# Performance work log

Hardware: AMD Instinct MI355X
Metric: run time of the kernel (lower is better)

Reference implementation:

```python
import jax, jax.numpy as jnp
import numpy as np

# Static config (matches init_kwargs / docstring example)
SHAPES = ((100, 100), (50, 50), (25, 25), (13, 13))  # (H, W) per level
L, P, NH, HD, E, F = 4, 4, 8, 32, 256, 1024
NUM_LAYERS = 6
EPS = 1e-5
NUM_KEYS = sum(h * w for h, w in SHAPES)  # 13294


def _ln(x, g, b):
    m = jnp.mean(x, -1, keepdims=True)
    v = jnp.var(x, -1, keepdims=True)
    return (x - m) * jax.lax.rsqrt(v + EPS) * g + b


def _ms_deform_attn(value, loc, aw):
    # value: (B,N,NH,HD)  loc: (B,N,NH,L,P,2) normalized  aw: (B,N,NH,L,P)
    B, N = value.shape[:2]
    out = jnp.zeros((B, NH, N, HD), value.dtype)
    start = 0
    for lvl, (h, w) in enumerate(SHAPES):
        v = value[:, start:start + h * w].transpose(0, 2, 1, 3)  # (B,NH,hw,HD)
        start += h * w
        # grid_sample align_corners=False pixel coords
        x = loc[:, :, :, lvl, :, 0] * w - 0.5  # (B,N,NH,P)
        y = loc[:, :, :, lvl, :, 1] * h - 0.5
        x0 = jnp.floor(x); y0 = jnp.floor(y)
        lx = x - x0; ly = y - y0
        x0 = x0.astype(jnp.int32); y0 = y0.astype(jnp.int32)

        def gather(yi, xi):
            valid = ((xi >= 0) & (xi < w) & (yi >= 0) & (yi < h)).astype(value.dtype)
            idx = jnp.clip(yi, 0, h - 1) * w + jnp.clip(xi, 0, w - 1)  # (B,N,NH,P)
            idx = idx.transpose(0, 2, 1, 3).reshape(B, NH, N * P, 1)
            got = jnp.take_along_axis(v, idx, axis=2).reshape(B, NH, N, P, HD)
            return got * valid.transpose(0, 2, 1, 3)[..., None]

        def wgt(a):  # (B,N,NH,P) -> (B,NH,N,P,1)
            return a.transpose(0, 2, 1, 3)[..., None]

        samp = (gather(y0, x0) * wgt((1 - lx) * (1 - ly))
                + gather(y0, x0 + 1) * wgt(lx * (1 - ly))
                + gather(y0 + 1, x0) * wgt((1 - lx) * ly)
                + gather(y0 + 1, x0 + 1) * wgt(lx * ly))  # (B,NH,N,P,HD)
        out = out + jnp.sum(samp * wgt(aw[:, :, :, lvl]), axis=3)
    return out.transpose(0, 2, 1, 3).reshape(B, N, NH * HD)


def _layer(x, ref, Woff, boff, Waw, baw, Wv, bv, Wo, bo, ln1_g, ln1_b, Wf1, bf1, Wf2, bf2, ln2_g, ln2_b):
    B, N, _ = x.shape
    v = (x @ Wv + bv).reshape(B, N, NH, HD)
    off = (x @ Woff + boff).reshape(B, N, NH, L, P, 2)
    aw = jax.nn.softmax((x @ Waw + baw).reshape(B, N, NH, L * P), -1).reshape(B, N, NH, L, P)
    normalizer = jnp.asarray([[w, h] for (h, w) in SHAPES], x.dtype)  # (L,2) in (x,y)=(W,H)
    loc = ref[:, :, None, :, None, :] + off / normalizer[None, None, None, :, None, :]
    attn = _ms_deform_attn(v, loc, aw) @ Wo + bo
    x = _ln(x + attn, ln1_g, ln1_b)
    f = jax.nn.relu(x @ Wf1 + bf1) @ Wf2 + bf2
    return _ln(x + f, ln2_g, ln2_b)


def setup_inputs() -> dict:
    key = jax.random.key(0)
    ks = jax.random.split(key, 10)
    s = 0.02
    return {
        "src": jax.random.normal(ks[0], (2, NUM_KEYS, E), jnp.float32),
        "reference_points": jax.random.uniform(ks[1], (2, NUM_KEYS, L, 2), jnp.float32),
        "spatial_shapes": jnp.asarray(SHAPES, jnp.int32),
        "level_start_index": jnp.asarray([0, 10000, 12500, 13125], jnp.int32),
        "Woff": jax.random.normal(ks[2], (E, NH * L * P * 2), jnp.float32) * s,
        "boff": jnp.zeros((NH * L * P * 2,), jnp.float32),
        "Waw": jax.random.normal(ks[3], (E, NH * L * P), jnp.float32) * s,
        "baw": jnp.zeros((NH * L * P,), jnp.float32),
        "Wv": jax.random.normal(ks[4], (E, E), jnp.float32) * s,
        "bv": jnp.zeros((E,), jnp.float32),
        "Wo": jax.random.normal(ks[5], (E, E), jnp.float32) * s,
        "bo": jnp.zeros((E,), jnp.float32),
        "ln1_g": jnp.ones((E,), jnp.float32),
        "ln1_b": jnp.zeros((E,), jnp.float32),
        "Wf1": jax.random.normal(ks[6], (E, F), jnp.float32) * s,
        "bf1": jnp.zeros((F,), jnp.float32),
        "Wf2": jax.random.normal(ks[7], (F, E), jnp.float32) * s,
        "bf2": jnp.zeros((E,), jnp.float32),
        "ln2_g": jnp.ones((E,), jnp.float32),
        "ln2_b": jnp.zeros((E,), jnp.float32),
    }


def reference(src, reference_points, spatial_shapes, level_start_index, Woff, boff, Waw, baw, Wv, bv, Wo, bo, ln1_g, ln1_b, Wf1, bf1, Wf2, bf2, ln2_g, ln2_b):
    # NOTE: the torch encoder reuses the SAME layer object num_layers times,
    # so parameters are shared across all 6 layers.
    x = src
    for _ in range(NUM_LAYERS):
        x = _layer(x, reference_points, Woff, boff, Waw, baw, Wv, bv, Wo, bo,
                   ln1_g, ln1_b, Wf1, bf1, Wf2, bf2, ln2_g, ln2_b)
    return x
```

## Files before the change

### kernel.cpp

```cpp
#include <hip/hip_runtime.h>
#include <hip/hip_bf16.h>
#include <math.h>

#define NKEYS 13294
#define BATCH 2
#define MROWS (BATCH * NKEYS)
#define EDIM  256
#define FDIM  1024
#define EPSV  1e-5f

typedef __bf16 bf16x8 __attribute__((ext_vector_type(8)));
typedef float  f32x4  __attribute__((ext_vector_type(4)));
typedef float  f32x2  __attribute__((ext_vector_type(2)));

__device__ __forceinline__ void async16(const void* g, void* l) {
    __builtin_amdgcn_global_load_lds(
        (const __attribute__((address_space(1))) void*)g,
        (__attribute__((address_space(3))) void*)l, 16, 0, 0);
}

template<int MODE>
__global__ __launch_bounds__(256, 4) void gemm_mfma_k(
    const __hip_bfloat16* __restrict__ A, const __hip_bfloat16* __restrict__ WT,
    const float* __restrict__ bias, __hip_bfloat16* __restrict__ Cout,
    int M, int N, int K,
    __hip_bfloat16* __restrict__ o_vb, __hip_bfloat16* __restrict__ o_off,
    __hip_bfloat16* __restrict__ o_aw)
{
    constexpr int BM = 128, BN = 128, BKc = 32;
    constexpr int SMX = (BM + BN) * BKc;
    __shared__ __hip_bfloat16 smem[2 * SMX];

    const int gx = gridDim.x, nb = gx * gridDim.y;
    int bxi = blockIdx.x, byi = blockIdx.y;
    if ((nb & 7) == 0) {
        const int id   = byi * gx + bxi;
        const int tile = (id & 7) * (nb >> 3) + (id >> 3);
        bxi = tile % gx; byi = tile / gx;
    }
    const int bm = byi * BM;
    const int bn = bxi * BN;

    const int tid  = threadIdx.x;
    const int lane = tid & 63;
    const int w    = tid >> 6;
    const int wr   = w >> 1, wc = w & 1;
    const int l15  = lane & 15, quad = lane >> 4;

    const int gRow = tid >> 2;
    const int kc8  = (tid & 3) * 8;
    const __hip_bfloat16* gsrc[4];
    int ldsoff[4];
    #pragma unroll
    for (int rr = 0; rr < 4; ++rr) {
        const int gr = gRow + 64 * rr;
        if (gr < BM) {
            int ar = bm + gr; if (ar >= M) ar = M - 1;
            gsrc[rr] = A + (size_t)ar * K + kc8;
        } else {
            gsrc[rr] = WT + (size_t)(bn + gr - BM) * K + kc8;
        }
        ldsoff[rr] = gr * BKc + kc8;
    }

    f32x4 acc[4][4];
    #pragma unroll
    for (int i = 0; i < 4; ++i)
        #pragma unroll
        for (int j = 0; j < 4; ++j) acc[i][j] = (f32x4)0.f;

    const int T = K / BKc;
    #pragma unroll
    for (int rr = 0; rr < 4; ++rr) async16(gsrc[rr], smem + ldsoff[rr]);

    for (int it = 0; it < T; ++it) {
        __syncthreads();
        if (it + 1 < T) {
            const int nxt = ((it + 1) & 1) * SMX;
            const int ko  = (it + 1) * BKc;
            #pragma unroll
            for (int rr = 0; rr < 4; ++rr) async16(gsrc[rr] + ko, smem + nxt + ldsoff[rr]);
        }
        const __hip_bfloat16* sA = smem + (it & 1) * SMX;
        const __hip_bfloat16* sB = sA + BM * BKc;

        bf16x8 a[4], b[4];
        #pragma unroll
        for (int mt = 0; mt < 4; ++mt)
            a[mt] = *(const bf16x8*)&sA[(wr * 64 + mt * 16 + l15) * BKc + quad * 8];
        #pragma unroll
        for (int nt = 0; nt < 4; ++nt)
            b[nt] = *(const bf16x8*)&sB[(wc * 64 + nt * 16 + l15) * BKc + quad * 8];
        #pragma unroll
        for (int mt = 0; mt < 4; ++mt)
            #pragma unroll
            for (int nt = 0; nt < 4; ++nt)
                acc[mt][nt] = __builtin_amdgcn_mfma_f32_16x16x32_bf16(
                    b[nt], a[mt], acc[mt][nt], 0, 0, 0);
    }

    #pragma unroll
    for (int nt = 0; nt < 4; ++nt) {
        const int col = bn + wc * 64 + nt * 16 + quad * 4;
        const float4 bz = *(const float4*)&bias[col];
        #pragma unroll
        for (int mt = 0; mt < 4; ++mt) {
            const int row = bm + wr * 64 + mt * 16 + l15;
            if (row >= M) continue;
            float v0 = acc[mt][nt][0] + bz.x;
            float v1 = acc[mt][nt][1] + bz.y;
            float v2 = acc[mt][nt][2] + bz.z;
            float v3 = acc[mt][nt][3] + bz.w;
            if (MODE == 3) {
                v0 = fmaxf(v0, 0.f); v1 = fmaxf(v1, 0.f);
                v2 = fmaxf(v2, 0.f); v3 = fmaxf(v3, 0.f);
            }
            union { uint2 u; __hip_bfloat16 h[4]; } p;
            p.h[0] = __float2bfloat16(v0); p.h[1] = __float2bfloat16(v1);
            p.h[2] = __float2bfloat16(v2); p.h[3] = __float2bfloat16(v3);
            if (MODE == 1) {
                if (col < 256) {
                    const int bb = (row >= NKEYS) ? 1 : 0;
                    const int hh = col >> 5, d = col & 31;
                    *(uint2*)&o_vb[((size_t)(bb * 7 + hh) * NKEYS + row) * 32 + d] = p.u;
                } else if (col < 512) {
                    *(uint2*)&o_off[(size_t)row * 256 + (col - 256)] = p.u;
                } else {
                    *(uint2*)&o_aw[(size_t)row * 128 + (col - 512)] = p.u;
                }
            } else {
                *(uint2*)&Cout[(size_t)row * N + col] = p.u;
            }
        }
    }
}

template<int FINAL>
__global__ __launch_bounds__(256, 2) void gemm_ln_k(
    const __hip_bfloat16* __restrict__ A, const __hip_bfloat16* __restrict__ WT,
    const float* __restrict__ bias, const __hip_bfloat16* __restrict__ xres,
    const float* __restrict__ g, const float* __restrict__ bta,
    float* __restrict__ xfout, __hip_bfloat16* __restrict__ xbout,
    int M, int K)
{
    constexpr int BM = 64, BN = 256, BKc = 32;
    constexpr int ROWS = BM + BN;
    constexpr int SLAB = ROWS * BKc;
    constexpr int SMX  = 2 * SLAB;
    __shared__ __hip_bfloat16 smem[2 * SMX];

    const int tid  = threadIdx.x;
    const int bm   = blockIdx.x * BM;
    const int lane = tid & 63;
    const int w    = tid >> 6;
    const int l15  = lane & 15, quad = lane >> 4;

    const int gRow = tid >> 2;
    const int kc8  = (tid & 3) * 8;
    const __hip_bfloat16* gsrc[5];
    int ldsoff[5];
    #pragma unroll
    for (int rr = 0; rr < 5; ++rr) {
        const int gr = gRow + 64 * rr;
        if (gr < BM) {
            int ar = bm + gr; if (ar >= M) ar = M - 1;
            gsrc[rr] = A + (size_t)ar * K + kc8;
        } else {
            gsrc[rr] = WT + (size_t)(gr - BM) * K + kc8;
        }
        ldsoff[rr] = gr * BKc + kc8;
    }

    f32x4 acc[4][4];
    #pragma unroll
    for (int i = 0; i < 4; ++i)
        #pragma unroll
        for (int j = 0; j < 4; ++j) acc[i][j] = (f32x4)0.f;

    const int T = K / 64;
    #pragma unroll
    for (int rr = 0; rr < 5; ++rr) {
        async16(gsrc[rr],      smem + ldsoff[rr]);
        async16(gsrc[rr] + 32, smem + SLAB + ldsoff[rr]);
    }

    for (int it = 0; it < T; ++it) {
        __syncthreads();
        if (it + 1 < T) {
            const int nxt = ((it + 1) & 1) * SMX;
            const int ko  = (it + 1) * 64;
            #pragma unroll
            for (int rr = 0; rr < 5; ++rr) {
                async16(gsrc[rr] + ko,      smem + nxt + ldsoff[rr]);
                async16(gsrc[rr] + ko + 32, smem + nxt + SLAB + ldsoff[rr]);
            }
        }
        #pragma unroll
        for (int s = 0; s < 2; ++s) {
            const __hip_bfloat16* sA = smem + (it & 1) * SMX + s * SLAB;
            const __hip_bfloat16* sB = sA + BM * BKc;

            bf16x8 a[4], b[4];
            #pragma unroll
            for (int mt = 0; mt < 4; ++mt)
                a[mt] = *(const bf16x8*)&sA[(mt * 16 + l15) * BKc + quad * 8];
            #pragma unroll
            for (int nt = 0; nt < 4; ++nt)
                b[nt] = *(const bf16x8*)&sB[(w * 64 + nt * 16 + l15) * BKc + quad * 8];
            #pragma unroll
            for (int mt = 0; mt < 4; ++mt)
                #pragma unroll
                for (int nt = 0; nt < 4; ++nt)
                    acc[mt][nt] = __builtin_amdgcn_mfma_f32_16x16x32_bf16(
                        b[nt], a[mt], acc[mt][nt], 0, 0, 0);
        }
    }

    const int colq = w * 64 + quad * 4;

    #pragma unroll
    for (int nt = 0; nt < 4; ++nt) {
        const int col = colq + nt * 16;
        const float4 bz = *(const float4*)&bias[col];
        #pragma unroll
        for (int mt = 0; mt < 4; ++mt) {
            int row = bm + mt * 16 + l15;
            if (row >= M) row = M - 1;
            const ushort4 xr = *(const ushort4*)&xres[(size_t)row * 256 + col];
            acc[mt][nt][0] += bz.x + __uint_as_float((unsigned)xr.x << 16);
            acc[mt][nt][1] += bz.y + __uint_as_float((unsigned)xr.y << 16);
            acc[mt][nt][2] += bz.z + __uint_as_float((unsigned)xr.z << 16);
            acc[mt][nt][3] += bz.w + __uint_as_float((unsigned)xr.w << 16);
        }
    }

    __syncthreads();
    float* stats = (float*)smem;
    #pragma unroll
    for (int mt = 0; mt < 4; ++mt) {
        float s = 0.f, sq = 0.f;
        #pragma unroll
        for (int nt = 0; nt < 4; ++nt)
            #pragma unroll
            for (int r = 0; r < 4; ++r) {
                const float v = acc[mt][nt][r];
                s += v; sq += v * v;
            }
        s  += __shfl_xor(s,  16, 64);  s  += __shfl_xor(s,  32, 64);
        sq += __shfl_xor(sq, 16, 64);  sq += __shfl_xor(sq, 32, 64);
        if (quad == 0) {
            const int rl = mt * 16 + l15;
            stats[(w * 64 + rl) * 2 + 0] = s;
            stats[(w * 64 + rl) * 2 + 1] = sq;
        }
    }
    __syncthreads();

    #pragma unroll
    for (int mt = 0; mt < 4; ++mt) {
        const int rl  = mt * 16 + l15;
        const int row = bm + rl;
        float s  = stats[rl * 2]          + stats[(64 + rl) * 2]
                 + stats[(128 + rl) * 2]  + stats[(192 + rl) * 2];
        float sq = stats[rl * 2 + 1]      + stats[(64 + rl) * 2 + 1]
                 + stats[(128 + rl) * 2 + 1] + stats[(192 + rl) * 2 + 1];
        const float mean = s * (1.f / 256.f);
        const float var  = sq * (1.f / 256.f) - mean * mean;
        const float rstd = rsqrtf(var + EPSV);
        if (row < M) {
            #pragma unroll
            for (int nt = 0; nt < 4; ++nt) {
                const int col = colq + nt * 16;
                const float4 gz  = *(const float4*)&g[col];
                const float4 bb4 = *(const float4*)&bta[col];
                const float v0 = (acc[mt][nt][0] - mean) * rstd * gz.x + bb4.x;
                const float v1 = (acc[mt][nt][1] - mean) * rstd * gz.y + bb4.y;
                const float v2 = (acc[mt][nt][2] - mean) * rstd * gz.z + bb4.z;
                const float v3 = (acc[mt][nt][3] - mean) * rstd * gz.w + bb4.w;
                union { uint2 u; __hip_bfloat16 h[4]; } p;
                p.h[0] = __float2bfloat16(v0); p.h[1] = __float2bfloat16(v1);
                p.h[2] = __float2bfloat16(v2); p.h[3] = __float2bfloat16(v3);
                *(uint2*)&xbout[(size_t)row * 256 + col] = p.u;
                if (FINAL) {
                    float4 f; f.x = v0; f.y = v1; f.z = v2; f.w = v3;
                    *(float4*)&xfout[(size_t)row * 256 + col] = f;
                }
            }
        }
    }
}

#define NB_SRC  6647
#define NB_WV   256
#define NB_WOFF 256
#define NB_WAW  128
#define NB_WO   256
#define NB_WF1  1024
#define NB_WF2  1024
#define NB_BIAS 3
#define NB_PREP (NB_SRC + NB_WV + NB_WOFF + NB_WAW + NB_WO + NB_WF1 + NB_WF2 + NB_BIAS)

__global__ void prep_k(
    const float* __restrict__ src,  __hip_bfloat16* __restrict__ xb,
    const float* __restrict__ Wv,   const float* __restrict__ Woff,
    const float* __restrict__ Waw,  const float* __restrict__ Wo,
    const float* __restrict__ Wf1,  const float* __restrict__ Wf2,
    const float* __restrict__ bv,   const float* __restrict__ boff,
    const float* __restrict__ baw,
    __hip_bfloat16* __restrict__ WT1, __hip_bfloat16* __restrict__ WTo,
    __hip_bfloat16* __restrict__ WTf1, __hip_bfloat16* __restrict__ WTf2,
    float* __restrict__ bias1)
{
    int b = blockIdx.x;
    const int t = threadIdx.x;

    if (b < NB_SRC) {
        const int i = b * 256 + t;
        const float4 v = ((const float4*)src)[i];
        xb[i * 4 + 0] = __float2bfloat16(v.x);
        xb[i * 4 + 1] = __float2bfloat16(v.y);
        xb[i * 4 + 2] = __float2bfloat16(v.z);
        xb[i * 4 + 3] = __float2bfloat16(v.w);
        return;
    }
    b -= NB_SRC;

    const float* W; __hip_bfloat16* WT; int N, rowOff;
    if (b < NB_WV)        { W = Wv;   WT = WT1;  N = 256;  rowOff = 0;   }
    else if ((b -= NB_WV)   < NB_WOFF) { W = Woff; WT = WT1;  N = 256;  rowOff = 256; }
    else if ((b -= NB_WOFF) < NB_WAW)  { W = Waw;  WT = WT1;  N = 128;  rowOff = 512; }
    else if ((b -= NB_WAW)  < NB_WO)   { W = Wo;   WT = WTo;  N = 256;  rowOff = 0;   }
    else if ((b -= NB_WO)   < NB_WF1)  { W = Wf1;  WT = WTf1; N = 1024; rowOff = 0;   }
    else if ((b -= NB_WF1)  < NB_WF2)  { W = Wf2;  WT = WTf2; N = 256;  rowOff = 0;   }
    else {
        b -= NB_WF2;
        const int i = b * 256 + t;
        if (i < 256) bias1[i] = bv[i];
        else if (i < 512) bias1[i] = boff[i - 256];
        else if (i < 640) bias1[i] = baw[i - 512];
        return;
    }
    const int idx = b * 256 + t;
    const int k = idx / N, n = idx % N;
    const int K = (WT == WTf2) ? 1024 : 256;
    WT[(size_t)(rowOff + n) * K + k] = __float2bfloat16(W[idx]);
}

__global__ __launch_bounds__(256) void sample_k(
    const __hip_bfloat16* __restrict__ v_bf,
    const __hip_bfloat16* __restrict__ offb,
    const __hip_bfloat16* __restrict__ awb,
    const float* __restrict__ ref,
    __hip_bfloat16* __restrict__ out)
{
    __shared__ alignas(16) float sw[272][4];
    __shared__ alignas(16) int   sa[272][4];
    const int t  = threadIdx.x;
    const int q0 = blockIdx.x * 2;
    const int qi = t >> 7, h = (t >> 4) & 7;

    {
        const int i = t & 15;
        const int q = q0 + qi;
        const int l = i >> 2;
        const float logit = __bfloat162float(awb[(size_t)q * 128 + h * 16 + i]);
        float mx = logit;
        #pragma unroll
        for (int m = 1; m < 16; m <<= 1) mx = fmaxf(mx, __shfl_xor(mx, m, 64));
        const float e = __expf(logit - mx);
        float s = e;
        #pragma unroll
        for (int m = 1; m < 16; m <<= 1) s += __shfl_xor(s, m, 64);
        const float aw = e / s;

        const int ww = (l == 0) ? 100 : (l == 1) ? 50 : (l == 2) ? 25 : 13;
        const int ls = (l == 0) ? 0 : (l == 1) ? 10000 : (l == 2) ? 12500 : 13125;
        const int b  = (q >= NKEYS) ? 1 : 0;
        const int slab = (b * 8 + h) * NKEYS + ls;

        const __hip_bfloat162 ofp = *(const __hip_bfloat162*)&offb[(size_t)q * 256 + h * 32 + i * 2];
        const float2 rf = *(const float2*)&ref[(size_t)q * 8 + l * 2];
        const float x = rf.x * (float)ww + __bfloat162float(ofp.x) - 0.5f;
        const float y = rf.y * (float)ww + __bfloat162float(ofp.y) - 0.5f;
        const float x0f = floorf(x), y0f = floorf(y);
        const float lx = x - x0f, ly = y - y0f;
        const int x0 = (int)x0f, y0 = (int)y0f;
        const bool x0ok = (x0 >= 0) & (x0 < ww);
        const bool x1ok = (x0 + 1 >= 0) & (x0 + 1 < ww);
        const bool y0ok = (y0 >= 0) & (y0 < ww);
        const bool y1ok = (y0 + 1 >= 0) & (y0 + 1 < ww);

        float w00 = (1.f - lx) * (1.f - ly) * aw;
        float w01 = lx * (1.f - ly) * aw;
        float w10 = (1.f - lx) * ly * aw;
        float w11 = lx * ly * aw;
        int a00 = slab + y0 * ww + x0;
        int a01 = a00 + 1;
        int a10 = a00 + ww;
        int a11 = a10 + 1;
        if (!(y0ok & x0ok)) { w00 = 0.f; a00 = 0; }
        if (!(y0ok & x1ok)) { w01 = 0.f; a01 = 0; }
        if (!(y1ok & x0ok)) { w10 = 0.f; a10 = 0; }
        if (!(y1ok & x1ok)) { w11 = 0.f; a11 = 0; }

        const int idx = (qi * 8 + h) * 17 + i;
        sw[idx][0] = w00; sw[idx][1] = w01; sw[idx][2] = w10; sw[idx][3] = w11;
        sa[idx][0] = a00 * 64; sa[idx][1] = a01 * 64;
        sa[idx][2] = a10 * 64; sa[idx][3] = a11 * 64;
    }
    __syncthreads();

    const int d2 = t & 15;
    const unsigned d4 = d2 * 4;
    const char* vb = (const char*)v_bf;
    const int ebase = (qi * 8 + h) * 17;
    f32x2 acc = (f32x2)0.f;
    #pragma unroll
    for (int i = 0; i < 16; ++i) {
        const f32x4 wv = *(const f32x4*)sw[ebase + i];
        const int4  av = *(const int4*)sa[ebase + i];
        const unsigned p0 = *(const unsigned*)(vb + ((unsigned)av.x + d4));
        const unsigned p1 = *(const unsigned*)(vb + ((unsigned)av.y + d4));
        const unsigned p2 = *(const unsigned*)(vb + ((unsigned)av.z + d4));
        const unsigned p3 = *(const unsigned*)(vb + ((unsigned)av.w + d4));
        f32x2 v;
        v[0] = __uint_as_float(p0 << 16); v[1] = __uint_as_float(p0 & 0xffff0000u);
        acc += (f32x2)(wv[0]) * v;
        v[0] = __uint_as_float(p1 << 16); v[1] = __uint_as_float(p1 & 0xffff0000u);
        acc += (f32x2)(wv[1]) * v;
        v[0] = __uint_as_float(p2 << 16); v[1] = __uint_as_float(p2 & 0xffff0000u);
        acc += (f32x2)(wv[2]) * v;
        v[0] = __uint_as_float(p3 << 16); v[1] = __uint_as_float(p3 & 0xffff0000u);
        acc += (f32x2)(wv[3]) * v;
    }
    __hip_bfloat162 ov;
    ov.x = __float2bfloat16(acc[0]);
    ov.y = __float2bfloat16(acc[1]);
    *(__hip_bfloat162*)&out[(size_t)(q0 + qi) * 256 + h * 32 + d2 * 2] = ov;
}

extern "C" void kernel_launch(void* const* d_in, const int* in_sizes, int n_in,
                              void* d_out, int out_size, void* d_ws, size_t ws_size,
                              hipStream_t stream)
{
    const float* src  = (const float*)d_in[0];
    const float* ref  = (const float*)d_in[1];
    const float* Woff = (const float*)d_in[4];
    const float* boff = (const float*)d_in[5];
    const float* Waw  = (const float*)d_in[6];
    const float* baw  = (const float*)d_in[7];
    const float* Wv   = (const float*)d_in[8];
    const float* bv   = (const float*)d_in[9];
    const float* Wo   = (const float*)d_in[10];
    const float* bo   = (const float*)d_in[11];
    const float* ln1g = (const float*)d_in[12];
    const float* ln1b = (const float*)d_in[13];
    const float* Wf1  = (const float*)d_in[14];
    const float* bf1  = (const float*)d_in[15];
    const float* Wf2  = (const float*)d_in[16];
    const float* bf2  = (const float*)d_in[17];
    const float* ln2g = (const float*)d_in[18];
    const float* ln2b = (const float*)d_in[19];

    float* x = (float*)d_out;

    float* ws = (float*)d_ws;
    float* bias1 = ws;
    __hip_bfloat16* v_bf  = (__hip_bfloat16*)(bias1 + 640);
    __hip_bfloat16* offb  = v_bf  + (size_t)MROWS * 256;
    __hip_bfloat16* awb   = offb  + (size_t)MROWS * 256;
    __hip_bfloat16* xb    = awb   + (size_t)MROWS * 128;
    __hip_bfloat16* attnb = xb    + (size_t)MROWS * 256;
    __hip_bfloat16* hb    = attnb + (size_t)MROWS * 256;
    __hip_bfloat16* WT1   = hb    + (size_t)MROWS * 1024;
    __hip_bfloat16* WTo   = WT1   + 640 * 256;
    __hip_bfloat16* WTf1  = WTo   + 256 * 256;
    __hip_bfloat16* WTf2  = WTf1  + 1024 * 256;

    prep_k<<<NB_PREP, 256, 0, stream>>>(
        src, xb, Wv, Woff, Waw, Wo, Wf1, Wf2, bv, boff, baw,
        WT1, WTo, WTf1, WTf2, bias1);

    const int gy  = (MROWS + 127) / 128;
    const int gln = (MROWS + 63) / 64;
    for (int layer = 0; layer < 6; ++layer) {
        gemm_mfma_k<1><<<dim3(640 / 128, gy), 256, 0, stream>>>(
            xb, WT1, bias1, nullptr, MROWS, 640, 256, v_bf, offb, awb);
        sample_k<<<MROWS / 2, 256, 0, stream>>>(v_bf, offb, awb, ref, attnb);
        gemm_ln_k<0><<<gln, 256, 0, stream>>>(
            attnb, WTo, bo, xb, ln1g, ln1b, nullptr, xb, MROWS, 256);
        gemm_mfma_k<3><<<dim3(1024 / 128, gy), 256, 0, stream>>>(
            xb, WTf1, bf1, hb, MROWS, 1024, 256, nullptr, nullptr, nullptr);
        if (layer < 5)
            gemm_ln_k<0><<<gln, 256, 0, stream>>>(
                hb, WTf2, bf2, xb, ln2g, ln2b, nullptr, xb, MROWS, 1024);
        else
            gemm_ln_k<1><<<gln, 256, 0, stream>>>(
                hb, WTf2, bf2, xb, ln2g, ln2b, x, xb, MROWS, 1024);
    }
}
```

Measured before the change: 993.9 us.

## Fuse attention-weight softmax into projection GEMM epilogue; widen LN GEMM to 8 waves

The softmax over attention logits moves from the sampling kernel into the epilogue of the fused value/offset/weight projection GEMM. The GEMM now writes normalized weights, so the sampler just loads them and skips its shuffle reductions. Separately, the GEMM+LayerNorm kernel now runs 512 threads as a 2x4 wave grid with half the accumulators per wave, aiming for more latency hiding and occupancy. The risk is register pressure from the new epilogue and a changed LDS load mapping that must stay correct.

```diff
diff --git a/kernel.cpp b/kernel.cpp
--- a/kernel.cpp
+++ b/kernel.cpp
@@ -97,6 +97,40 @@
             for (int nt = 0; nt < 4; ++nt)
                 acc[mt][nt] = __builtin_amdgcn_mfma_f32_16x16x32_bf16(
                     b[nt], a[mt], acc[mt][nt], 0, 0, 0);
+    }
+
+    if (MODE == 1 && bn == 512) {
+        #pragma unroll
+        for (int nt = 0; nt < 4; ++nt) {
+            const int col = 512 + wc * 64 + nt * 16 + quad * 4;
+            const float4 bz = *(const float4*)&bias[col];
+            #pragma unroll
+            for (int mt = 0; mt < 4; ++mt) {
+                const int row = bm + wr * 64 + mt * 16 + l15;
+                const float v0 = acc[mt][nt][0] + bz.x;
+                const float v1 = acc[mt][nt][1] + bz.y;
+                const float v2 = acc[mt][nt][2] + bz.z;
+                const float v3 = acc[mt][nt][3] + bz.w;
+                float mx = fmaxf(fmaxf(v0, v1), fmaxf(v2, v3));
+                mx = fmaxf(mx, __shfl_xor(mx, 16, 64));
+                mx = fmaxf(mx, __shfl_xor(mx, 32, 64));
+                const float e0 = __expf(v0 - mx), e1 = __expf(v1 - mx);
+                const float e2 = __expf(v2 - mx), e3 = __expf(v3 - mx);
+                float s = e0 + e1 + e2 + e3;
+                s += __shfl_xor(s, 16, 64);
+                s += __shfl_xor(s, 32, 64);
+                const float rs = 1.f / s;
+                if (row < M) {
+                    union { uint2 u; __hip_bfloat16 h[4]; } p;
+                    p.h[0] = __float2bfloat16(e0 * rs);
+                    p.h[1] = __float2bfloat16(e1 * rs);
+                    p.h[2] = __float2bfloat16(e2 * rs);
+                    p.h[3] = __float2bfloat16(e3 * rs);
+                    *(uint2*)&o_aw[(size_t)row * 128 + (col - 512)] = p.u;
+                }
+            }
+        }
+        return;
     }
 
     #pragma unroll
@@ -123,10 +157,8 @@
                     const int bb = (row >= NKEYS) ? 1 : 0;
                     const int hh = col >> 5, d = col & 31;
                     *(uint2*)&o_vb[((size_t)(bb * 7 + hh) * NKEYS + row) * 32 + d] = p.u;
-                } else if (col < 512) {
+                } else {
                     *(uint2*)&o_off[(size_t)row * 256 + (col - 256)] = p.u;
-                } else {
-                    *(uint2*)&o_aw[(size_t)row * 128 + (col - 512)] = p.u;
                 }
             } else {
                 *(uint2*)&Cout[(size_t)row * N + col] = p.u;
@@ -136,7 +168,7 @@
 }
 
 template<int FINAL>
-__global__ __launch_bounds__(256, 2) void gemm_ln_k(
+__global__ __launch_bounds__(512, 4) void gemm_ln_k(
     const __hip_bfloat16* __restrict__ A, const __hip_bfloat16* __restrict__ WT,
     const float* __restrict__ bias, const __hip_bfloat16* __restrict__ xres,
     const float* __restrict__ g, const float* __restrict__ bta,
@@ -153,36 +185,37 @@
     const int bm   = blockIdx.x * BM;
     const int lane = tid & 63;
     const int w    = tid >> 6;
+    const int wr   = w >> 2;
+    const int wc   = w & 3;
     const int l15  = lane & 15, quad = lane >> 4;
 
-    const int gRow = tid >> 2;
-    const int kc8  = (tid & 3) * 8;
     const __hip_bfloat16* gsrc[5];
     int ldsoff[5];
     #pragma unroll
     for (int rr = 0; rr < 5; ++rr) {
-        const int gr = gRow + 64 * rr;
+        const int idx = rr * 512 + tid;
+        const int rG  = idx >> 2;
+        const int kcc = (idx & 3) * 8;
+        const int sl  = (rG >= 320) ? 1 : 0;
+        const int gr  = rG - sl * 320;
         if (gr < BM) {
             int ar = bm + gr; if (ar >= M) ar = M - 1;
-            gsrc[rr] = A + (size_t)ar * K + kc8;
+            gsrc[rr] = A + (size_t)ar * K + sl * 32 + kcc;
         } else {
-            gsrc[rr] = WT + (size_t)(gr - BM) * K + kc8;
-        }
-        ldsoff[rr] = gr * BKc + kc8;
-    }
-
-    f32x4 acc[4][4];
-    #pragma unroll
-    for (int i = 0; i < 4; ++i)
+            gsrc[rr] = WT + (size_t)(gr - BM) * K + sl * 32 + kcc;
+        }
+        ldsoff[rr] = idx * 8;
+    }
+
+    f32x4 acc[2][4];
+    #pragma unroll
+    for (int i = 0; i < 2; ++i)
         #pragma unroll
         for (int j = 0; j < 4; ++j) acc[i][j] = (f32x4)0.f;
 
     const int T = K / 64;
     #pragma unroll
-    for (int rr = 0; rr < 5; ++rr) {
-        async16(gsrc[rr],      smem + ldsoff[rr]);
-        async16(gsrc[rr] + 32, smem + SLAB + ldsoff[rr]);
-    }
+    for (int rr = 0; rr < 5; ++rr) async16(gsrc[rr], smem + ldsoff[rr]);
 
     for (int it = 0; it < T; ++it) {
         __syncthreads();
@@ -190,25 +223,23 @@
             const int nxt = ((it + 1) & 1) * SMX;
             const int ko  = (it + 1) * 64;
             #pragma unroll
-            for (int rr = 0; rr < 5; ++rr) {
-                async16(gsrc[rr] + ko,      smem + nxt + ldsoff[rr]);
-                async16(gsrc[rr] + ko + 32, smem + nxt + SLAB + ldsoff[rr]);
-            }
+            for (int rr = 0; rr < 5; ++rr)
+                async16(gsrc[rr] + ko, smem + nxt + ldsoff[rr]);
         }
         #pragma unroll
         for (int s = 0; s < 2; ++s) {
             const __hip_bfloat16* sA = smem + (it & 1) * SMX + s * SLAB;
             const __hip_bfloat16* sB = sA + BM * BKc;
 
-            bf16x8 a[4], b[4];
-            #pragma unroll
-            for (int mt = 0; mt < 4; ++mt)
-                a[mt] = *(const bf16x8*)&sA[(mt * 16 + l15) * BKc + quad * 8];
+            bf16x8 a[2], b[4];
+            #pragma unroll
+            for (int mt = 0; mt < 2; ++mt)
+                a[mt] = *(const bf16x8*)&sA[(wr * 32 + mt * 16 + l15) * BKc + quad * 8];
             #pragma unroll
             for (int nt = 0; nt < 4; ++nt)
-                b[nt] = *(const bf16x8*)&sB[(w * 64 + nt * 16 + l15) * BKc + quad * 8];
-            #pragma unroll
-            for (int mt = 0; mt < 4; ++mt)
+                b[nt] = *(const bf16x8*)&sB[(wc * 64 + nt * 16 + l15) * BKc + quad * 8];
+            #pragma unroll
+            for (int mt = 0; mt < 2; ++mt)
                 #pragma unroll
                 for (int nt = 0; nt < 4; ++nt)
                     acc[mt][nt] = __builtin_amdgcn_mfma_f32_16x16x32_bf16(
@@ -216,15 +247,15 @@
         }
     }
 
-    const int colq = w * 64 + quad * 4;
+    const int colq = wc * 64 + quad * 4;
 
     #pragma unroll
     for (int nt = 0; nt < 4; ++nt) {
         const int col = colq + nt * 16;
         const float4 bz = *(const float4*)&bias[col];
         #pragma unroll
-        for (int mt = 0; mt < 4; ++mt) {
-            int row = bm + mt * 16 + l15;
+        for (int mt = 0; mt < 2; ++mt) {
+            int row = bm + wr * 32 + mt * 16 + l15;
             if (row >= M) row = M - 1;
             const ushort4 xr = *(const ushort4*)&xres[(size_t)row * 256 + col];
             acc[mt][nt][0] += bz.x + __uint_as_float((unsigned)xr.x << 16);
@@ -237,7 +268,7 @@
     __syncthreads();
     float* stats = (float*)smem;
     #pragma unroll
-    for (int mt = 0; mt < 4; ++mt) {
+    for (int mt = 0; mt < 2; ++mt) {
         float s = 0.f, sq = 0.f;
         #pragma unroll
         for (int nt = 0; nt < 4; ++nt)
@@ -249,16 +280,16 @@
         s  += __shfl_xor(s,  16, 64);  s  += __shfl_xor(s,  32, 64);
         sq += __shfl_xor(sq, 16, 64);  sq += __shfl_xor(sq, 32, 64);
         if (quad == 0) {
-            const int rl = mt * 16 + l15;
-            stats[(w * 64 + rl) * 2 + 0] = s;
-            stats[(w * 64 + rl) * 2 + 1] = sq;
+            const int rl = wr * 32 + mt * 16 + l15;
+            stats[(wc * 64 + rl) * 2 + 0] = s;
+            stats[(wc * 64 + rl) * 2 + 1] = sq;
         }
     }
     __syncthreads();
 
     #pragma unroll
-    for (int mt = 0; mt < 4; ++mt) {
-        const int rl  = mt * 16 + l15;
+    for (int mt = 0; mt < 2; ++mt) {
+        const int rl  = wr * 32 + mt * 16 + l15;
         const int row = bm + rl;
         float s  = stats[rl * 2]          + stats[(64 + rl) * 2]
                  + stats[(128 + rl) * 2]  + stats[(192 + rl) * 2];
@@ -363,15 +394,7 @@
         const int i = t & 15;
         const int q = q0 + qi;
         const int l = i >> 2;
-        const float logit = __bfloat162float(awb[(size_t)q * 128 + h * 16 + i]);
-        float mx = logit;
-        #pragma unroll
-        for (int m = 1; m < 16; m <<= 1) mx = fmaxf(mx, __shfl_xor(mx, m, 64));
-        const float e = __expf(logit - mx);
-        float s = e;
-        #pragma unroll
-        for (int m = 1; m < 16; m <<= 1) s += __shfl_xor(s, m, 64);
-        const float aw = e / s;
+        const float aw = __bfloat162float(awb[(size_t)q * 128 + h * 16 + i]);
 
         const int ww = (l == 0) ? 100 : (l == 1) ? 50 : (l == 2) ? 25 : 13;
         const int ls = (l == 0) ? 0 : (l == 1) ? 10000 : (l == 2) ? 12500 : 13125;
@@ -487,15 +510,15 @@
         gemm_mfma_k<1><<<dim3(640 / 128, gy), 256, 0, stream>>>(
             xb, WT1, bias1, nullptr, MROWS, 640, 256, v_bf, offb, awb);
         sample_k<<<MROWS / 2, 256, 0, stream>>>(v_bf, offb, awb, ref, attnb);
-        gemm_ln_k<0><<<gln, 256, 0, stream>>>(
+        gemm_ln_k<0><<<gln, 512, 0, stream>>>(
             attnb, WTo, bo, xb, ln1g, ln1b, nullptr, xb, MROWS, 256);
         gemm_mfma_k<3><<<dim3(1024 / 128, gy), 256, 0, stream>>>(
             xb, WTf1, bf1, hb, MROWS, 1024, 256, nullptr, nullptr, nullptr);
         if (layer < 5)
-            gemm_ln_k<0><<<gln, 256, 0, stream>>>(
+            gemm_ln_k<0><<<gln, 512, 0, stream>>>(
                 hb, WTf2, bf2, xb, ln2g, ln2b, nullptr, xb, MROWS, 1024);
         else
-            gemm_ln_k<1><<<gln, 256, 0, stream>>>(
+            gemm_ln_k<1><<<gln, 512, 0, stream>>>(
                 hb, WTf2, bf2, xb, ln2g, ln2b, x, xb, MROWS, 1024);
     }
 }
```

After: 1.064 ms. 1.07x slower.
